# Optimization experiments

Measured on AMD Instinct MI355X. Metric: run time of the kernel, lower is better.

The kernel has to match this reference:

```python
import jax, jax.numpy as jnp
import numpy as np

EPS = 1e-5

def _bn(h, gamma, beta):
    # BatchNorm1d in training mode: biased batch stats over the batch dim
    m = h.mean(axis=0)
    v = h.var(axis=0)
    return gamma * (h - m) * jax.lax.rsqrt(v + EPS) + beta


def setup_inputs() -> dict:
    key = jax.random.key(0)
    ks = jax.random.split(key, 8)
    N, E, D = 100000, 1000000, 64
    x = jax.random.normal(ks[0], (N, D), dtype=jnp.float32)
    pair_features = jax.random.normal(ks[1], (E, D), dtype=jnp.float32)
    pair_index = jax.random.randint(ks[2], (2, E), 0, N, dtype=jnp.int32)
    s = 1.0 / np.sqrt(D)
    W_atom = jax.random.uniform(ks[3], (D, D), jnp.float32, -s, s)
    b_atom = jnp.zeros((D,), jnp.float32)
    g_atom = jnp.ones((D,), jnp.float32)
    be_atom = jnp.zeros((D,), jnp.float32)
    W_pair = jax.random.uniform(ks[4], (D, D), jnp.float32, -s, s)
    b_pair = jnp.zeros((D,), jnp.float32)
    g_pair = jnp.ones((D,), jnp.float32)
    be_pair = jnp.zeros((D,), jnp.float32)
    s2 = 1.0 / np.sqrt(2 * D)
    W_a2p = jax.random.uniform(ks[5], (2 * D, D), jnp.float32, -s2, s2)
    b_a2p = jnp.zeros((D,), jnp.float32)
    return {
        "x": x, "pair_features": pair_features, "pair_index": pair_index,
        "W_atom": W_atom, "b_atom": b_atom, "g_atom": g_atom, "be_atom": be_atom,
        "W_pair": W_pair, "b_pair": b_pair, "g_pair": g_pair, "be_pair": be_pair,
        "W_a2p": W_a2p, "b_a2p": b_a2p,
    }


def reference(x, pair_features, pair_index,
              W_atom, b_atom, g_atom, be_atom,
              W_pair, b_pair, g_pair, be_pair,
              W_a2p, b_a2p):
    # atom path: Linear -> ReLU -> BatchNorm
    atom_out = _bn(jax.nn.relu(x @ W_atom + b_atom), g_atom, be_atom)
    # pair path: gather send/recv atoms, concat, linear
    send = x[pair_index[0]]                       # [E, D]
    recv = x[pair_index[1]]                       # [E, D]
    pair_input = jnp.concatenate([send, recv], axis=-1)  # [E, 2D]
    a2p = pair_input @ W_a2p + b_a2p              # [E, Dp]
    pair_bn = _bn(jax.nn.relu(pair_features @ W_pair + b_pair), g_pair, be_pair)
    return atom_out, a2p + pair_bn
```

## Files before the change

### kernel.cpp

```cpp
#include <hip/hip_runtime.h>

#define D 64
#define EPS 1e-5f

typedef __bf16 bf16x4 __attribute__((ext_vector_type(4)));
typedef __bf16 bf16x8 __attribute__((ext_vector_type(8)));
typedef float  f32x4  __attribute__((ext_vector_type(4)));

#define MFMA(a, b, c) __builtin_amdgcn_mfma_f32_16x16x32_bf16((a), (b), (c), 0, 0, 0)

static inline int imin(int a, int b) { return a < b ? a : b; }

#define LDS_STRIDE 80

template <bool NTLOAD>
__global__ void __launch_bounds__(256) fused_h_stats_kernel(
    const float* __restrict__ in, const float* __restrict__ W,
    const float* __restrict__ bias, int nrows,
    float* __restrict__ stats, __bf16* __restrict__ hout)
{
    __shared__ __bf16 lds[4][32 * LDS_STRIDE];
    const int tid = threadIdx.x;
    const int lane = tid & 63, wv = tid >> 6;
    const int q = lane >> 4, l16 = lane & 15;
    __bf16* my = lds[wv];

    bf16x8 Bf[2][4];
#pragma unroll
    for (int ks = 0; ks < 2; ++ks)
#pragma unroll
      for (int nt = 0; nt < 4; ++nt)
#pragma unroll
        for (int j = 0; j < 8; ++j)
          Bf[ks][nt][j] = (__bf16)W[(ks * 32 + q * 8 + j) * 64 + nt * 16 + l16];

    float bc[4];
#pragma unroll
    for (int nt = 0; nt < 4; ++nt) bc[nt] = bias[nt * 16 + l16];

    float s[4] = {0.f, 0.f, 0.f, 0.f}, sq[4] = {0.f, 0.f, 0.f, 0.f};
    const f32x4 ZERO = {0.f, 0.f, 0.f, 0.f};

    const int ntiles = (nrows + 31) >> 5;
    const int stride = gridDim.x << 2;

    auto LOADTILE = [&](int tt, f32x4* ld) {
        const int row0 = tt << 5;
        if (row0 + 32 <= nrows) {
            const float* tb = in + (size_t)row0 * 64 + lane * 4;
#pragma unroll
            for (int i = 0; i < 8; ++i)
                ld[i] = NTLOAD ? __builtin_nontemporal_load((const f32x4*)(tb + i * 256))
                               : *(const f32x4*)(tb + i * 256);
        } else {
#pragma unroll
            for (int i = 0; i < 8; ++i) {
                int row = row0 + i * 4 + (lane >> 4);
                ld[i] = (row < nrows)
                          ? *(const f32x4*)(in + (size_t)row * 64 + (lane & 15) * 4)
                          : ZERO;
            }
        }
    };

    int t = (blockIdx.x << 2) + wv;
    bool valid = t < ntiles;
    f32x4 ld[8];
    if (valid) LOADTILE(t, ld);

    while (valid) {
        bf16x4 c[8];
#pragma unroll
        for (int i = 0; i < 8; ++i)
#pragma unroll
          for (int j = 0; j < 4; ++j)
            c[i][j] = (__bf16)ld[i][j];

        const int tn = t + stride;
        const bool vn = tn < ntiles;
        if (vn) LOADTILE(tn, ld);

#pragma unroll
        for (int i = 0; i < 8; ++i) {
            int wrow = i * 4 + (lane >> 4);
            *(bf16x4*)&my[wrow * LDS_STRIDE + (lane & 15) * 4] = c[i];
        }

        bf16x8 af[2][2];
#pragma unroll
        for (int mt = 0; mt < 2; ++mt)
#pragma unroll
          for (int ks = 0; ks < 2; ++ks)
            af[mt][ks] = *(const bf16x8*)&my[(mt * 16 + l16) * LDS_STRIDE + ks * 32 + q * 8];

        f32x4 acc[2][4];
#pragma unroll
        for (int mt = 0; mt < 2; ++mt)
#pragma unroll
          for (int nt = 0; nt < 4; ++nt) {
            acc[mt][nt] = MFMA(af[mt][0], Bf[0][nt], ZERO);
            acc[mt][nt] = MFMA(af[mt][1], Bf[1][nt], acc[mt][nt]);
          }

#pragma unroll
        for (int mt = 0; mt < 2; ++mt) {
            bf16x8 hh[2];
#pragma unroll
            for (int nt = 0; nt < 4; ++nt)
#pragma unroll
              for (int r = 0; r < 4; ++r) {
                const int row = (t << 5) + mt * 16 + q * 4 + r;
                float h = fmaxf(acc[mt][nt][r] + bc[nt], 0.f);
                if (row < nrows) { s[nt] += h; sq[nt] = fmaf(h, h, sq[nt]); }
                hh[nt >> 1][(nt & 1) * 4 + r] = (__bf16)h;
              }
            if (((2 * t + mt) << 4) < nrows) {
                __bf16* dst = hout + ((size_t)(2 * t + mt) * 2048 + lane * 16);
                *(bf16x8*)dst = hh[0];
                *(bf16x8*)(dst + 8) = hh[1];
            }
        }

        t = tn; valid = vn;
    }

#pragma unroll
    for (int nt = 0; nt < 4; ++nt) {
        s[nt]  += __shfl_xor(s[nt], 16, 64);  s[nt]  += __shfl_xor(s[nt], 32, 64);
        sq[nt] += __shfl_xor(sq[nt], 16, 64); sq[nt] += __shfl_xor(sq[nt], 32, 64);
    }
    if (q == 0) {
#pragma unroll
        for (int nt = 0; nt < 4; ++nt) {
            atomicAdd(&stats[nt * 16 + l16], s[nt]);
            atomicAdd(&stats[64 + nt * 16 + l16], sq[nt]);
        }
    }
}

__global__ void finalize_stats_kernel(
    const float* __restrict__ stats,
    const float* __restrict__ g_a, const float* __restrict__ be_a,
    const float* __restrict__ g_p, const float* __restrict__ be_p,
    float n_atom, float n_pair, float* __restrict__ params)
{
    const int t = threadIdx.x;
    const int j = t & 63;
    const bool p = t >= 64;
    const float* st = stats + (p ? 128 : 0);
    const float* g  = p ? g_p  : g_a;
    const float* be = p ? be_p : be_a;
    const float cnt = p ? n_pair : n_atom;
    float m = st[j] / cnt;
    float v = st[64 + j] / cnt - m * m;
    float sc = g[j] * rsqrtf(v + EPS);
    float sh = be[j] - m * sc;
    float* pr = params + (p ? 128 : 0);
    pr[j] = sc;
    pr[64 + j] = sh;
}

__global__ void __launch_bounds__(256) apply_atom_kernel(
    float* __restrict__ out, const float* __restrict__ params, int nrows)
{
    const int tid = threadIdx.x;
    const int lane = tid & 63, wv = tid >> 6;
    const int q = lane >> 4, l16 = lane & 15;

    float sc[4], sh[4];
#pragma unroll
    for (int nt = 0; nt < 4; ++nt) {
        sc[nt] = params[nt * 16 + l16];
        sh[nt] = params[64 + nt * 16 + l16];
    }

    const int ntiles = (nrows + 15) >> 4;
    const int stride = gridDim.x << 2;
    for (int t = (blockIdx.x << 2) + wv; t < ntiles; t += stride) {
        const __bf16* src = (const __bf16*)out + ((size_t)t * 2048 + lane * 16);
        bf16x8 h0 = *(const bf16x8*)src;
        bf16x8 h1 = *(const bf16x8*)(src + 8);
        asm volatile("s_waitcnt vmcnt(0)" ::: "memory");
#pragma unroll
        for (int nt = 0; nt < 4; ++nt)
#pragma unroll
          for (int r = 0; r < 4; ++r) {
            const int row = (t << 4) + q * 4 + r;
            float h = (float)((nt < 2) ? h0[nt * 4 + r] : h1[(nt - 2) * 4 + r]);
            if (row < nrows)
                __builtin_nontemporal_store(fmaf(h, sc[nt], sh[nt]),
                                            out + (size_t)row * 64 + nt * 16 + l16);
          }
    }
}

__global__ void __launch_bounds__(256) pair_pass2_kernel(
    float* __restrict__ out, const float* __restrict__ x,
    const int* __restrict__ pidx,
    const float* __restrict__ Wa, const float* __restrict__ ba,
    int E, const float* __restrict__ params)
{
    const int tid = threadIdx.x;
    const int lane = tid & 63, wv = tid >> 6;
    const int q = lane >> 4, l16 = lane & 15;

    bf16x8 B2[4][4];
#pragma unroll
    for (int ks = 0; ks < 4; ++ks)
#pragma unroll
      for (int nt = 0; nt < 4; ++nt)
#pragma unroll
        for (int j = 0; j < 8; ++j)
          B2[ks][nt][j] = (__bf16)Wa[(ks * 32 + q * 8 + j) * 64 + nt * 16 + l16];

    float bac[4], sc[4], sh[4];
#pragma unroll
    for (int nt = 0; nt < 4; ++nt) {
        bac[nt] = ba[nt * 16 + l16];
        sc[nt]  = params[nt * 16 + l16];
        sh[nt]  = params[64 + nt * 16 + l16];
    }

    const f32x4 ZERO = {0.f, 0.f, 0.f, 0.f};

    const int ntiles = E >> 4;
    const int stride = gridDim.x << 2;
    for (int t = (blockIdx.x << 2) + wv; t < ntiles; t += stride) {
        const int e0 = t << 4;
        const int se = pidx[e0 + l16];
        const int re = pidx[E + e0 + l16];
        const float* ps = x + (size_t)se * 64 + q * 8;
        const float* pr = x + (size_t)re * 64 + q * 8;

        f32x4 g[4][2];
        g[0][0] = *(const f32x4*)ps;          g[0][1] = *(const f32x4*)(ps + 4);
        g[1][0] = *(const f32x4*)(ps + 32);   g[1][1] = *(const f32x4*)(ps + 36);
        g[2][0] = *(const f32x4*)pr;          g[2][1] = *(const f32x4*)(pr + 4);
        g[3][0] = *(const f32x4*)(pr + 32);   g[3][1] = *(const f32x4*)(pr + 36);

        const __bf16* hsrc = (const __bf16*)out + ((size_t)t * 2048 + lane * 16);
        bf16x8 h0 = *(const bf16x8*)hsrc;
        bf16x8 h1 = *(const bf16x8*)(hsrc + 8);

        bf16x8 af[4];
#pragma unroll
        for (int ks = 0; ks < 4; ++ks)
#pragma unroll
          for (int j = 0; j < 8; ++j)
            af[ks][j] = (__bf16)g[ks][j >> 2][j & 3];

        f32x4 acc[4];
#pragma unroll
        for (int nt = 0; nt < 4; ++nt) acc[nt] = ZERO;
#pragma unroll
        for (int ks = 0; ks < 4; ++ks)
#pragma unroll
          for (int nt = 0; nt < 4; ++nt)
            acc[nt] = MFMA(af[ks], B2[ks][nt], acc[nt]);

        asm volatile("s_waitcnt vmcnt(0)" ::: "memory");
#pragma unroll
        for (int nt = 0; nt < 4; ++nt)
#pragma unroll
          for (int r = 0; r < 4; ++r) {
            float h = (float)((nt < 2) ? h0[nt * 4 + r] : h1[(nt - 2) * 4 + r]);
            float val = fmaf(h, sc[nt], sh[nt]) + acc[nt][r] + bac[nt];
            __builtin_nontemporal_store(val,
                out + (size_t)(e0 + q * 4 + r) * 64 + nt * 16 + l16);
          }
    }
}

extern "C" void kernel_launch(void* const* d_in, const int* in_sizes, int n_in,
                              void* d_out, int out_size, void* d_ws, size_t ws_size,
                              hipStream_t stream) {
    const float* x       = (const float*)d_in[0];
    const float* pf      = (const float*)d_in[1];
    const int*   pidx    = (const int*)d_in[2];
    const float* W_atom  = (const float*)d_in[3];
    const float* b_atom  = (const float*)d_in[4];
    const float* g_atom  = (const float*)d_in[5];
    const float* be_atom = (const float*)d_in[6];
    const float* W_pair  = (const float*)d_in[7];
    const float* b_pair  = (const float*)d_in[8];
    const float* g_pair  = (const float*)d_in[9];
    const float* be_pair = (const float*)d_in[10];
    const float* W_a2p   = (const float*)d_in[11];
    const float* b_a2p   = (const float*)d_in[12];

    const int N = in_sizes[0] / D;
    const int E = in_sizes[1] / D;

    float* out_atom = (float*)d_out;
    float* out_pair = out_atom + (size_t)N * D;

    float* stats  = (float*)d_ws;
    float* params = stats + 256;

    (void)hipMemsetAsync(d_ws, 0, 256 * sizeof(float), stream);

    const int ta = (N + 31) / 32, tp = (E + 31) / 32;
    const int ga = imin((ta + 3) / 4, 1024);
    const int gp = imin((tp + 3) / 4, 1024);

    fused_h_stats_kernel<false><<<ga, 256, 0, stream>>>(
        x, W_atom, b_atom, N, stats, (__bf16*)out_atom);
    fused_h_stats_kernel<true><<<gp, 256, 0, stream>>>(
        pf, W_pair, b_pair, E, stats + 128, (__bf16*)out_pair);

    finalize_stats_kernel<<<1, 128, 0, stream>>>(stats, g_atom, be_atom,
                                                 g_pair, be_pair,
                                                 (float)N, (float)E, params);

    const int t16a = (N + 15) / 16, t16p = E / 16;
    apply_atom_kernel<<<imin((t16a + 3) / 4, 2048), 256, 0, stream>>>(
        out_atom, params, N);
    pair_pass2_kernel<<<imin((t16p + 3) / 4, 2048), 256, 0, stream>>>(
        out_pair, x, pidx, W_a2p, b_a2p, E, params + 128);
}
```

Before: 721.9 us.

## Merge atom/pair passes into single launches and software-pipeline pair gather

The atom and pair pass-1 kernels become one launch whose blocks are split proportionally between the two problems, and the same is done for the apply and pair pass-2 kernels. This removes launch gaps and tail underutilisation. When the workspace is large enough, the bf16 intermediate h goes to a compact workspace buffer instead of in place in the output, which lets the vmcnt(0) wait be dropped. The pair pass-2 loop now prefetches the next tile's indices, gather rows and h values while the current tile's MFMAs run, at the cost of more registers.

Result: no change. 715.6 us (-0.9%).

```diff
diff --git a/kernel.cpp b/kernel.cpp
--- a/kernel.cpp
+++ b/kernel.cpp
@@ -10,16 +10,29 @@
 #define MFMA(a, b, c) __builtin_amdgcn_mfma_f32_16x16x32_bf16((a), (b), (c), 0, 0, 0)
 
 static inline int imin(int a, int b) { return a < b ? a : b; }
+static inline int imax(int a, int b) { return a > b ? a : b; }
 
 #define LDS_STRIDE 80
 
-template <bool NTLOAD>
-__global__ void __launch_bounds__(256) fused_h_stats_kernel(
-    const float* __restrict__ in, const float* __restrict__ W,
-    const float* __restrict__ bias, int nrows,
-    float* __restrict__ stats, __bf16* __restrict__ hout)
+__global__ void __launch_bounds__(256) pass1_kernel(
+    const float* __restrict__ xA, const float* __restrict__ WA,
+    const float* __restrict__ bA, int NA,
+    const float* __restrict__ xP, const float* __restrict__ WP,
+    const float* __restrict__ bP, int NP,
+    float* __restrict__ stats, __bf16* __restrict__ hA, __bf16* __restrict__ hP,
+    int hstride, int atomBlocks)
 {
     __shared__ __bf16 lds[4][32 * LDS_STRIDE];
+    const bool isA = (int)blockIdx.x < atomBlocks;
+    const float* in   = isA ? xA : xP;
+    const float* W    = isA ? WA : WP;
+    const float* bias = isA ? bA : bP;
+    const int nrows   = isA ? NA : NP;
+    float* st         = stats + (isA ? 0 : 128);
+    __bf16* hout      = isA ? hA : hP;
+    const int bid     = isA ? blockIdx.x : blockIdx.x - atomBlocks;
+    const int nblk    = isA ? atomBlocks : gridDim.x - atomBlocks;
+
     const int tid = threadIdx.x;
     const int lane = tid & 63, wv = tid >> 6;
     const int q = lane >> 4, l16 = lane & 15;
@@ -42,7 +55,7 @@
     const f32x4 ZERO = {0.f, 0.f, 0.f, 0.f};
 
     const int ntiles = (nrows + 31) >> 5;
-    const int stride = gridDim.x << 2;
+    const int stride = nblk << 2;
 
     auto LOADTILE = [&](int tt, f32x4* ld) {
         const int row0 = tt << 5;
@@ -50,8 +63,7 @@
             const float* tb = in + (size_t)row0 * 64 + lane * 4;
 #pragma unroll
             for (int i = 0; i < 8; ++i)
-                ld[i] = NTLOAD ? __builtin_nontemporal_load((const f32x4*)(tb + i * 256))
-                               : *(const f32x4*)(tb + i * 256);
+                ld[i] = __builtin_nontemporal_load((const f32x4*)(tb + i * 256));
         } else {
 #pragma unroll
             for (int i = 0; i < 8; ++i) {
@@ -63,7 +75,7 @@
         }
     };
 
-    int t = (blockIdx.x << 2) + wv;
+    int t = (bid << 2) + wv;
     bool valid = t < ntiles;
     f32x4 ld[8];
     if (valid) LOADTILE(t, ld);
@@ -115,7 +127,7 @@
                 hh[nt >> 1][(nt & 1) * 4 + r] = (__bf16)h;
               }
             if (((2 * t + mt) << 4) < nrows) {
-                __bf16* dst = hout + ((size_t)(2 * t + mt) * 2048 + lane * 16);
+                __bf16* dst = hout + ((size_t)(2 * t + mt) * hstride + lane * 16);
                 *(bf16x8*)dst = hh[0];
                 *(bf16x8*)(dst + 8) = hh[1];
             }
@@ -132,8 +144,8 @@
     if (q == 0) {
 #pragma unroll
         for (int nt = 0; nt < 4; ++nt) {
-            atomicAdd(&stats[nt * 16 + l16], s[nt]);
-            atomicAdd(&stats[64 + nt * 16 + l16], sq[nt]);
+            atomicAdd(&st[nt * 16 + l16], s[nt]);
+            atomicAdd(&st[64 + nt * 16 + l16], sq[nt]);
         }
     }
 }
@@ -160,49 +172,50 @@
     pr[64 + j] = sh;
 }
 
-__global__ void __launch_bounds__(256) apply_atom_kernel(
-    float* __restrict__ out, const float* __restrict__ params, int nrows)
+__global__ void __launch_bounds__(256) pass2_kernel(
+    float* __restrict__ outA, const __bf16* __restrict__ hA, int NA,
+    float* __restrict__ outP, const __bf16* __restrict__ hP, int EP,
+    const float* __restrict__ x, const int* __restrict__ pidx,
+    const float* __restrict__ Wa, const float* __restrict__ ba,
+    const float* __restrict__ params, int hstride, int atomBlocks, int inplace)
 {
+    const bool isA = (int)blockIdx.x < atomBlocks;
+    const int bid  = isA ? blockIdx.x : blockIdx.x - atomBlocks;
+    const int nblk = isA ? atomBlocks : gridDim.x - atomBlocks;
     const int tid = threadIdx.x;
     const int lane = tid & 63, wv = tid >> 6;
     const int q = lane >> 4, l16 = lane & 15;
-
+    const int stride = nblk << 2;
+    const f32x4 ZERO = {0.f, 0.f, 0.f, 0.f};
+
+    const float* pp = params + (isA ? 0 : 128);
     float sc[4], sh[4];
 #pragma unroll
     for (int nt = 0; nt < 4; ++nt) {
-        sc[nt] = params[nt * 16 + l16];
-        sh[nt] = params[64 + nt * 16 + l16];
-    }
-
-    const int ntiles = (nrows + 15) >> 4;
-    const int stride = gridDim.x << 2;
-    for (int t = (blockIdx.x << 2) + wv; t < ntiles; t += stride) {
-        const __bf16* src = (const __bf16*)out + ((size_t)t * 2048 + lane * 16);
-        bf16x8 h0 = *(const bf16x8*)src;
-        bf16x8 h1 = *(const bf16x8*)(src + 8);
-        asm volatile("s_waitcnt vmcnt(0)" ::: "memory");
-#pragma unroll
-        for (int nt = 0; nt < 4; ++nt)
-#pragma unroll
-          for (int r = 0; r < 4; ++r) {
-            const int row = (t << 4) + q * 4 + r;
-            float h = (float)((nt < 2) ? h0[nt * 4 + r] : h1[(nt - 2) * 4 + r]);
-            if (row < nrows)
-                __builtin_nontemporal_store(fmaf(h, sc[nt], sh[nt]),
-                                            out + (size_t)row * 64 + nt * 16 + l16);
-          }
-    }
-}
-
-__global__ void __launch_bounds__(256) pair_pass2_kernel(
-    float* __restrict__ out, const float* __restrict__ x,
-    const int* __restrict__ pidx,
-    const float* __restrict__ Wa, const float* __restrict__ ba,
-    int E, const float* __restrict__ params)
-{
-    const int tid = threadIdx.x;
-    const int lane = tid & 63, wv = tid >> 6;
-    const int q = lane >> 4, l16 = lane & 15;
+        sc[nt] = pp[nt * 16 + l16];
+        sh[nt] = pp[64 + nt * 16 + l16];
+    }
+
+    if (isA) {
+        const int ntiles = (NA + 15) >> 4;
+        for (int t = (bid << 2) + wv; t < ntiles; t += stride) {
+            const __bf16* src = hA + ((size_t)t * hstride + lane * 16);
+            bf16x8 h0 = *(const bf16x8*)src;
+            bf16x8 h1 = *(const bf16x8*)(src + 8);
+            if (inplace) asm volatile("s_waitcnt vmcnt(0)" ::: "memory");
+#pragma unroll
+            for (int nt = 0; nt < 4; ++nt)
+#pragma unroll
+              for (int r = 0; r < 4; ++r) {
+                const int row = (t << 4) + q * 4 + r;
+                float h = (float)((nt < 2) ? h0[nt * 4 + r] : h1[(nt - 2) * 4 + r]);
+                if (row < NA)
+                    __builtin_nontemporal_store(fmaf(h, sc[nt], sh[nt]),
+                                                outA + (size_t)row * 64 + nt * 16 + l16);
+              }
+        }
+        return;
+    }
 
     bf16x8 B2[4][4];
 #pragma unroll
@@ -213,61 +226,77 @@
         for (int j = 0; j < 8; ++j)
           B2[ks][nt][j] = (__bf16)Wa[(ks * 32 + q * 8 + j) * 64 + nt * 16 + l16];
 
-    float bac[4], sc[4], sh[4];
-#pragma unroll
-    for (int nt = 0; nt < 4; ++nt) {
-        bac[nt] = ba[nt * 16 + l16];
-        sc[nt]  = params[nt * 16 + l16];
-        sh[nt]  = params[64 + nt * 16 + l16];
-    }
-
-    const f32x4 ZERO = {0.f, 0.f, 0.f, 0.f};
-
-    const int ntiles = E >> 4;
-    const int stride = gridDim.x << 2;
-    for (int t = (blockIdx.x << 2) + wv; t < ntiles; t += stride) {
-        const int e0 = t << 4;
-        const int se = pidx[e0 + l16];
-        const int re = pidx[E + e0 + l16];
+    float bac[4];
+#pragma unroll
+    for (int nt = 0; nt < 4; ++nt) bac[nt] = ba[nt * 16 + l16];
+
+    auto GATHER = [&](f32x4 (*g)[2], int se, int re) {
         const float* ps = x + (size_t)se * 64 + q * 8;
         const float* pr = x + (size_t)re * 64 + q * 8;
-
-        f32x4 g[4][2];
-        g[0][0] = *(const f32x4*)ps;          g[0][1] = *(const f32x4*)(ps + 4);
-        g[1][0] = *(const f32x4*)(ps + 32);   g[1][1] = *(const f32x4*)(ps + 36);
-        g[2][0] = *(const f32x4*)pr;          g[2][1] = *(const f32x4*)(pr + 4);
-        g[3][0] = *(const f32x4*)(pr + 32);   g[3][1] = *(const f32x4*)(pr + 36);
-
-        const __bf16* hsrc = (const __bf16*)out + ((size_t)t * 2048 + lane * 16);
-        bf16x8 h0 = *(const bf16x8*)hsrc;
-        bf16x8 h1 = *(const bf16x8*)(hsrc + 8);
-
-        bf16x8 af[4];
-#pragma unroll
-        for (int ks = 0; ks < 4; ++ks)
-#pragma unroll
-          for (int j = 0; j < 8; ++j)
-            af[ks][j] = (__bf16)g[ks][j >> 2][j & 3];
-
+        g[0][0] = *(const f32x4*)ps;        g[0][1] = *(const f32x4*)(ps + 4);
+        g[1][0] = *(const f32x4*)(ps + 32); g[1][1] = *(const f32x4*)(ps + 36);
+        g[2][0] = *(const f32x4*)pr;        g[2][1] = *(const f32x4*)(pr + 4);
+        g[3][0] = *(const f32x4*)(pr + 32); g[3][1] = *(const f32x4*)(pr + 36);
+    };
+
+    const int ntiles = EP >> 4;
+    int t = (bid << 2) + wv;
+    if (t >= ntiles) return;
+
+    int se = pidx[(t << 4) + l16];
+    int re = pidx[EP + (t << 4) + l16];
+    int tn = t + stride;
+    bool vn = tn < ntiles;
+    int sen = 0, ren = 0;
+    if (vn) { sen = pidx[(tn << 4) + l16]; ren = pidx[EP + (tn << 4) + l16]; }
+
+    f32x4 g[4][2];
+    GATHER(g, se, re);
+    const __bf16* hs = hP + ((size_t)t * hstride + lane * 16);
+    bf16x8 hc0 = *(const bf16x8*)hs;
+    bf16x8 hc1 = *(const bf16x8*)(hs + 8);
+    bf16x8 hn0, hn1;
+
+    for (;;) {
         f32x4 acc[4];
 #pragma unroll
         for (int nt = 0; nt < 4; ++nt) acc[nt] = ZERO;
 #pragma unroll
-        for (int ks = 0; ks < 4; ++ks)
-#pragma unroll
-          for (int nt = 0; nt < 4; ++nt)
-            acc[nt] = MFMA(af[ks], B2[ks][nt], acc[nt]);
-
-        asm volatile("s_waitcnt vmcnt(0)" ::: "memory");
+        for (int ks = 0; ks < 4; ++ks) {
+            bf16x8 a;
+#pragma unroll
+            for (int j = 0; j < 8; ++j) a[j] = (__bf16)g[ks][j >> 2][j & 3];
+#pragma unroll
+            for (int nt = 0; nt < 4; ++nt) acc[nt] = MFMA(a, B2[ks][nt], acc[nt]);
+        }
+
+        if (vn) {
+            GATHER(g, sen, ren);
+            const __bf16* hsn = hP + ((size_t)tn * hstride + lane * 16);
+            hn0 = *(const bf16x8*)hsn;
+            hn1 = *(const bf16x8*)(hsn + 8);
+        }
+        const int tnn = tn + stride;
+        if (tnn < ntiles) {
+            sen = pidx[(tnn << 4) + l16];
+            ren = pidx[EP + (tnn << 4) + l16];
+        }
+
+        if (inplace) asm volatile("s_waitcnt vmcnt(0)" ::: "memory");
+        const int e0 = t << 4;
 #pragma unroll
         for (int nt = 0; nt < 4; ++nt)
 #pragma unroll
           for (int r = 0; r < 4; ++r) {
-            float h = (float)((nt < 2) ? h0[nt * 4 + r] : h1[(nt - 2) * 4 + r]);
+            float h = (float)((nt < 2) ? hc0[nt * 4 + r] : hc1[(nt - 2) * 4 + r]);
             float val = fmaf(h, sc[nt], sh[nt]) + acc[nt][r] + bac[nt];
             __builtin_nontemporal_store(val,
-                out + (size_t)(e0 + q * 4 + r) * 64 + nt * 16 + l16);
+                outP + (size_t)(e0 + q * 4 + r) * 64 + nt * 16 + l16);
           }
+
+        if (!vn) break;
+        t = tn; tn = tnn; vn = tnn < ntiles;
+        hc0 = hn0; hc1 = hn1;
     }
 }
 
@@ -297,24 +326,38 @@
     float* stats  = (float*)d_ws;
     float* params = stats + 256;
 
+    const size_t mA = (size_t)((N + 15) / 16), mP = (size_t)(E / 16);
+    const size_t need = 4096 + (mA + mP) * 2048;
+    __bf16* hA; __bf16* hP; int hstride, inplace;
+    if (ws_size >= need) {
+        hA = (__bf16*)((char*)d_ws + 4096);
+        hP = hA + mA * 1024;
+        hstride = 1024; inplace = 0;
+    } else {
+        hA = (__bf16*)out_atom;
+        hP = (__bf16*)out_pair;
+        hstride = 2048; inplace = 1;
+    }
+
     (void)hipMemsetAsync(d_ws, 0, 256 * sizeof(float), stream);
 
-    const int ta = (N + 31) / 32, tp = (E + 31) / 32;
-    const int ga = imin((ta + 3) / 4, 1024);
-    const int gp = imin((tp + 3) / 4, 1024);
-
-    fused_h_stats_kernel<false><<<ga, 256, 0, stream>>>(
-        x, W_atom, b_atom, N, stats, (__bf16*)out_atom);
-    fused_h_stats_kernel<true><<<gp, 256, 0, stream>>>(
-        pf, W_pair, b_pair, E, stats + 128, (__bf16*)out_pair);
+    const int tA = (N + 31) / 32, tP = (E + 31) / 32;
+    int aB = imax(1, (int)((long long)1792 * tA / (tA + tP)));
+    aB = imin(aB, imax(1, (tA + 3) / 4));
+    int pB = imin(1792 - aB, imax(1, (tP + 3) / 4));
+    pass1_kernel<<<aB + pB, 256, 0, stream>>>(
+        x, W_atom, b_atom, N, pf, W_pair, b_pair, E,
+        stats, hA, hP, hstride, aB);
 
     finalize_stats_kernel<<<1, 128, 0, stream>>>(stats, g_atom, be_atom,
                                                  g_pair, be_pair,
                                                  (float)N, (float)E, params);
 
     const int t16a = (N + 15) / 16, t16p = E / 16;
-    apply_atom_kernel<<<imin((t16a + 3) / 4, 2048), 256, 0, stream>>>(
-        out_atom, params, N);
-    pair_pass2_kernel<<<imin((t16p + 3) / 4, 2048), 256, 0, stream>>>(
-        out_pair, x, pidx, W_a2p, b_a2p, E, params + 128);
+    int aB2 = imax(1, (int)((long long)1920 * t16a / (t16a + 2 * (long long)t16p)));
+    aB2 = imin(aB2, imax(1, (t16a + 3) / 4));
+    int pB2 = imin(1920 - aB2, imax(1, (t16p + 3) / 4));
+    pass2_kernel<<<aB2 + pB2, 256, 0, stream>>>(
+        out_atom, hA, N, out_pair, hP, E,
+        x, pidx, W_a2p, b_a2p, params, hstride, aB2, inplace);
 }
```
